# Kernel tuning notes

Hardware: AMD Instinct MI355X
Metric: run time of the kernel (lower is better)

## Reference

```python
import jax, jax.numpy as jnp
import numpy as np

NUM_FIELDS = 32
EMBED = 64
ATTN = 64
BATCH = 2048

# all field pairs (i < j), NC2 = 496
_ROW, _COL = np.triu_indices(NUM_FIELDS, k=1)
ROW_IDX = jnp.asarray(_ROW, dtype=jnp.int32)
COL_IDX = jnp.asarray(_COL, dtype=jnp.int32)


def setup_inputs() -> dict:
    key = jax.random.key(0)
    k0, k1, k2 = jax.random.split(key, 3)
    inputs = jax.random.normal(k0, (BATCH, NUM_FIELDS, EMBED), dtype=jnp.float32)
    # Linear init ~ U(-1/sqrt(fan_in), 1/sqrt(fan_in)) style scale
    W1 = jax.random.normal(k1, (EMBED, ATTN), dtype=jnp.float32) / jnp.sqrt(float(EMBED))
    b1 = jnp.zeros((ATTN,), dtype=jnp.float32)
    w2 = jax.random.normal(k2, (ATTN, 1), dtype=jnp.float32) / jnp.sqrt(float(ATTN))
    b2 = jnp.zeros((1,), dtype=jnp.float32)
    return {"inputs": inputs, "W1": W1, "b1": b1, "w2": w2, "b2": b2}


def reference(inputs, W1, b1, w2, b2):
    # inner: (B, P, E) pairwise elementwise products of field embeddings
    inner = inputs[:, ROW_IDX, :] * inputs[:, COL_IDX, :]
    # tiny 2-layer MLP attention: (B, P, E) -> (B, P, A) -> (B, P, 1)
    h = jax.nn.relu(jnp.einsum('bpe,ea->bpa', inner, W1) + b1)
    logits = jnp.einsum('bpa,ao->bpo', h, w2) + b2          # (B, P, 1)
    attn_scores = jax.nn.softmax(logits, axis=1)            # softmax over pair dim
    # softmax-weighted sum over pairs -> (B, E), then (B, 1, E)
    outputs = jnp.sum(attn_scores * inner, axis=1)
    return outputs[:, None, :], attn_scores
```

## Files before the change

### kernel.cpp

```cpp
#include <hip/hip_runtime.h>
#include <math.h>

#define NF 32
#define NE 64
#define NA 64
#define NP 496

typedef __attribute__((ext_vector_type(8))) _Float16 f16x8;
typedef __attribute__((ext_vector_type(4))) _Float16 f16x4;
typedef __attribute__((ext_vector_type(4))) float    f32x4;

#define W1T_S 72
#define XT_S  40
#define WT_S  40

__global__ __launch_bounds__(256, 4) void afm_fwd(
    const float* __restrict__ x,
    const float* __restrict__ W1,
    const float* __restrict__ b1,
    const float* __restrict__ w2,
    const float* __restrict__ b2,
    float* __restrict__ out,
    float* __restrict__ attn,
    int B)
{
    const int tid   = threadIdx.x;
    const int lane  = tid & 63;
    const int wv    = tid >> 6;
    const int smp   = wv >> 1;
    const int sub   = wv & 1;
    const int nlane = lane & 15;
    const int g     = lane >> 4;

    __shared__ __align__(16) _Float16 W1t[64][W1T_S];
    __shared__ __align__(16) _Float16 xh[2][8][NF][8];
    __shared__ __align__(16) _Float16 xT[2][NE][XT_S];
    __shared__ __align__(16) _Float16 Wt[2][NF][WT_S];
    __shared__ float s_l[2][NP];
    __shared__ unsigned short s_rc[512];

    {
        const int e = tid & 63, a0 = (tid >> 6) << 4;
        const float* wr = W1 + e * NA + a0;
        #pragma unroll
        for (int i = 0; i < 4; ++i) {
            const float4 v = *(const float4*)(wr + 4 * i);
            W1t[a0 + 4*i + 0][e] = (_Float16)v.x;
            W1t[a0 + 4*i + 1][e] = (_Float16)v.y;
            W1t[a0 + 4*i + 2][e] = (_Float16)v.z;
            W1t[a0 + 4*i + 3][e] = (_Float16)v.w;
        }
    }
    for (int p = tid; p < 512; p += 256) {
        const int pp = (p < NP) ? p : NP - 1;
        const float sq = sqrtf((float)(3969 - 8 * pp));
        int r = (int)((63.0f - sq) * 0.5f);
        int st = (r * (63 - r)) >> 1;
        if (pp < st) { --r; st = (r * (63 - r)) >> 1; }
        else { const int st2 = ((r + 1) * (62 - r)) >> 1; if (pp >= st2) { ++r; st = st2; } }
        const int c = pp - st + r + 1;
        s_rc[p] = (unsigned short)(r | (c << 8));
    }

    int b = blockIdx.x * 2 + smp;
    if (b >= B) b = B - 1;

    {
        unsigned int* wz = (unsigned int*)&Wt[smp][0][0];
        #pragma unroll
        for (int i = 0; i < 5; ++i) {
            const int idx = i * 64 + lane;
            if (idx < 320) wz[sub * 320 + idx] = 0u;
        }
    }

    const float* __restrict__ xb = x + (size_t)b * (NF * NE);
    {
        const int r  = sub * 16 + (lane >> 2);
        const int e0 = (lane & 3) << 4;
        #pragma unroll
        for (int i = 0; i < 4; ++i) {
            const int e = e0 + 4 * i;
            const float4 v = *(const float4*)(xb + r * NE + e);
            f16x4 hv = { (_Float16)v.x, (_Float16)v.y, (_Float16)v.z, (_Float16)v.w };
            *(f16x4*)&xh[smp][e >> 3][r][e & 7] = hv;
            xT[smp][e + 0][r] = hv[0];
            xT[smp][e + 1][r] = hv[1];
            xT[smp][e + 2][r] = hv[2];
            xT[smp][e + 3][r] = hv[3];
        }
    }
    __syncthreads();

    f16x8 w1f[2][4];
    #pragma unroll
    for (int s = 0; s < 2; ++s)
        #pragma unroll
        for (int mt = 0; mt < 4; ++mt)
            w1f[s][mt] = *(const f16x8*)&W1t[mt * 16 + nlane][s * 32 + g * 8];

    f32x4 b1q[4], w2q[4];
    #pragma unroll
    for (int mt = 0; mt < 4; ++mt) {
        b1q[mt] = *(const f32x4*)(b1 + mt * 16 + g * 4);
        w2q[mt] = *(const f32x4*)(w2 + mt * 16 + g * 4);
    }
    const float bias2 = b2[0];

    const int t_end = sub ? 31 : 16;
    #pragma unroll 2
    for (int t = sub * 16; t < t_end; ++t) {
        const int p0 = t << 4;
        const unsigned short rc = s_rc[p0 + nlane];
        const int r = rc & 255, c = rc >> 8;

        f16x8 af[2];
        #pragma unroll
        for (int s = 0; s < 2; ++s) {
            const f16x8 xr8 = *(const f16x8*)&xh[smp][4 * s + g][r][0];
            const f16x8 xc8 = *(const f16x8*)&xh[smp][4 * s + g][c][0];
            af[s] = xr8 * xc8;
        }
        f32x4 acc[4];
        #pragma unroll
        for (int mt = 0; mt < 4; ++mt) acc[mt] = b1q[mt];
        #pragma unroll
        for (int s = 0; s < 2; ++s)
            #pragma unroll
            for (int mt = 0; mt < 4; ++mt)
                acc[mt] = __builtin_amdgcn_mfma_f32_16x16x32_f16(w1f[s][mt], af[s], acc[mt], 0, 0, 0);

        float logit = 0.0f;
        #pragma unroll
        for (int mt = 0; mt < 4; ++mt) {
            logit = fmaf(fmaxf(acc[mt][0], 0.0f), w2q[mt][0], logit);
            logit = fmaf(fmaxf(acc[mt][1], 0.0f), w2q[mt][1], logit);
            logit = fmaf(fmaxf(acc[mt][2], 0.0f), w2q[mt][2], logit);
            logit = fmaf(fmaxf(acc[mt][3], 0.0f), w2q[mt][3], logit);
        }
        logit += __shfl_xor(logit, 16);
        logit += __shfl_xor(logit, 32);
        if (lane < 16) s_l[smp][p0 + lane] = logit + bias2;
    }
    __syncthreads();

    float lv[8], mx = -1e30f;
    #pragma unroll
    for (int k = 0; k < 8; ++k) {
        const int p = (k << 6) + lane;
        lv[k] = (p < NP) ? s_l[smp][p] : -1e30f;
        mx = fmaxf(mx, lv[k]);
    }
    #pragma unroll
    for (int off = 1; off < 64; off <<= 1) mx = fmaxf(mx, __shfl_xor(mx, off));

    float ev[8], se = 0.0f;
    #pragma unroll
    for (int k = 0; k < 8; ++k) {
        const int p = (k << 6) + lane;
        ev[k] = (p < NP) ? __expf(lv[k] - mx) : 0.0f;
        se += ev[k];
    }
    #pragma unroll
    for (int off = 1; off < 64; off <<= 1) se += __shfl_xor(se, off);
    const float inv = 1.0f / se;

    float* __restrict__ attn_b = attn + (size_t)b * NP;
    #pragma unroll
    for (int k = 0; k < 4; ++k) {
        const int kk = (sub << 2) + k;
        const int p = (kk << 6) + lane;
        if (p < NP) {
            const float w = ev[kk] * inv;
            attn_b[p] = w;
            const unsigned short rc = s_rc[p];
            const int r = rc & 255, c = rc >> 8;
            const _Float16 wh = (_Float16)w;
            Wt[smp][r][c] = wh;
            Wt[smp][c][r] = wh;
        }
    }
    __syncthreads();

    f16x8 wa[2], xbf[2];
    #pragma unroll
    for (int mt = 0; mt < 2; ++mt)
        wa[mt] = *(const f16x8*)&Wt[smp][mt * 16 + nlane][g * 8];
    #pragma unroll
    for (int j = 0; j < 2; ++j) {
        const int nt = 2 * sub + j;
        xbf[j] = *(const f16x8*)&xT[smp][nt * 16 + nlane][g * 8];
    }

    f32x4 y[2][2];
    #pragma unroll
    for (int mt = 0; mt < 2; ++mt)
        #pragma unroll
        for (int j = 0; j < 2; ++j) {
            y[mt][j] = (f32x4)0.0f;
            y[mt][j] = __builtin_amdgcn_mfma_f32_16x16x32_f16(wa[mt], xbf[j], y[mt][j], 0, 0, 0);
        }

    float po[2] = {0.f, 0.f};
    #pragma unroll
    for (int j = 0; j < 2; ++j) {
        const int nt = 2 * sub + j;
        #pragma unroll
        for (int mt = 0; mt < 2; ++mt) {
            const f16x4 xv = *(const f16x4*)&xT[smp][nt * 16 + nlane][mt * 16 + g * 4];
            po[j] += (float)xv[0] * y[mt][j][0];
            po[j] += (float)xv[1] * y[mt][j][1];
            po[j] += (float)xv[2] * y[mt][j][2];
            po[j] += (float)xv[3] * y[mt][j][3];
        }
        po[j] += __shfl_xor(po[j], 16);
        po[j] += __shfl_xor(po[j], 32);
    }
    if (lane < 16) {
        float* __restrict__ ob = out + (size_t)b * NE;
        #pragma unroll
        for (int j = 0; j < 2; ++j)
            ob[(2 * sub + j) * 16 + lane] = 0.5f * po[j];
    }
}

extern "C" void kernel_launch(void* const* d_in, const int* in_sizes, int n_in,
                              void* d_out, int out_size, void* d_ws, size_t ws_size,
                              hipStream_t stream) {
    const float* x  = (const float*)d_in[0];
    const float* W1 = (const float*)d_in[1];
    const float* b1 = (const float*)d_in[2];
    const float* w2 = (const float*)d_in[3];
    const float* b2 = (const float*)d_in[4];

    const int B = in_sizes[0] / (NF * NE);
    float* out_p  = (float*)d_out;
    float* attn_p = (float*)d_out + (size_t)B * NE;

    afm_fwd<<<(B + 1) / 2, 256, 0, stream>>>(x, W1, b1, w2, b2, out_p, attn_p, B);
}
```

Measured before the change: 23.38 us.

## Compute pair indices incrementally per lane and fully unroll the logit loop

Each lane now handles a contiguous run of 31 pairs. It computes its starting (row, col) once and advances it incrementally, so each iteration no longer reads the index table from shared memory. The loop is fully unrolled with a guard, MFMA issue priority is raised with s_setprio, and the w2 dot product is split into four independent accumulators for more ILP. The strided logit writes (31*lane) to shared memory may cause bank conflicts, and full unrolling increases code size and register pressure.

```diff
diff --git a/kernel.cpp b/kernel.cpp
--- a/kernel.cpp
+++ b/kernel.cpp
@@ -90,6 +90,18 @@
             xT[smp][e + 3][r] = hv[3];
         }
     }
+
+    int pr, pc;
+    {
+        const int p0 = 31 * nlane + 16 * sub;
+        const float sq = sqrtf((float)(3969 - 8 * p0));
+        int r = (int)((63.0f - sq) * 0.5f);
+        int st = (r * (63 - r)) >> 1;
+        if (p0 < st) { --r; st = (r * (63 - r)) >> 1; }
+        else { const int st2 = ((r + 1) * (62 - r)) >> 1; if (p0 >= st2) { ++r; st = st2; } }
+        pr = r;
+        pc = p0 - st + r + 1;
+    }
     __syncthreads();
 
     f16x8 w1f[2][4];
@@ -107,40 +119,45 @@
     }
     const float bias2 = b2[0];
 
-    const int t_end = sub ? 31 : 16;
-    #pragma unroll 2
-    for (int t = sub * 16; t < t_end; ++t) {
-        const int p0 = t << 4;
-        const unsigned short rc = s_rc[p0 + nlane];
-        const int r = rc & 255, c = rc >> 8;
-
-        f16x8 af[2];
-        #pragma unroll
-        for (int s = 0; s < 2; ++s) {
-            const f16x8 xr8 = *(const f16x8*)&xh[smp][4 * s + g][r][0];
-            const f16x8 xc8 = *(const f16x8*)&xh[smp][4 * s + g][c][0];
-            af[s] = xr8 * xc8;
-        }
-        f32x4 acc[4];
-        #pragma unroll
-        for (int mt = 0; mt < 4; ++mt) acc[mt] = b1q[mt];
-        #pragma unroll
-        for (int s = 0; s < 2; ++s)
-            #pragma unroll
-            for (int mt = 0; mt < 4; ++mt)
-                acc[mt] = __builtin_amdgcn_mfma_f32_16x16x32_f16(w1f[s][mt], af[s], acc[mt], 0, 0, 0);
-
-        float logit = 0.0f;
-        #pragma unroll
-        for (int mt = 0; mt < 4; ++mt) {
-            logit = fmaf(fmaxf(acc[mt][0], 0.0f), w2q[mt][0], logit);
-            logit = fmaf(fmaxf(acc[mt][1], 0.0f), w2q[mt][1], logit);
-            logit = fmaf(fmaxf(acc[mt][2], 0.0f), w2q[mt][2], logit);
-            logit = fmaf(fmaxf(acc[mt][3], 0.0f), w2q[mt][3], logit);
-        }
-        logit += __shfl_xor(logit, 16);
-        logit += __shfl_xor(logit, 32);
-        if (lane < 16) s_l[smp][p0 + lane] = logit + bias2;
+    #pragma unroll
+    for (int t = 0; t < 16; ++t) {
+        if (16 * sub + t < 31) {
+            f16x8 af[2];
+            #pragma unroll
+            for (int s = 0; s < 2; ++s) {
+                const f16x8 xr8 = *(const f16x8*)&xh[smp][4 * s + g][pr][0];
+                const f16x8 xc8 = *(const f16x8*)&xh[smp][4 * s + g][pc][0];
+                af[s] = xr8 * xc8;
+            }
+            f32x4 acc[4];
+            #pragma unroll
+            for (int mt = 0; mt < 4; ++mt) acc[mt] = b1q[mt];
+            __builtin_amdgcn_s_setprio(1);
+            #pragma unroll
+            for (int s = 0; s < 2; ++s)
+                #pragma unroll
+                for (int mt = 0; mt < 4; ++mt)
+                    acc[mt] = __builtin_amdgcn_mfma_f32_16x16x32_f16(w1f[s][mt], af[s], acc[mt], 0, 0, 0);
+            __builtin_amdgcn_s_setprio(0);
+
+            float pl0 = 0.f, pl1 = 0.f, pl2 = 0.f, pl3 = 0.f;
+            #pragma unroll
+            for (int mt = 0; mt < 4; ++mt) {
+                pl0 = fmaf(fmaxf(acc[mt][0], 0.0f), w2q[mt][0], pl0);
+                pl1 = fmaf(fmaxf(acc[mt][1], 0.0f), w2q[mt][1], pl1);
+                pl2 = fmaf(fmaxf(acc[mt][2], 0.0f), w2q[mt][2], pl2);
+                pl3 = fmaf(fmaxf(acc[mt][3], 0.0f), w2q[mt][3], pl3);
+            }
+            float logit = (pl0 + pl1) + (pl2 + pl3);
+            logit += __shfl_xor(logit, 16);
+            logit += __shfl_xor(logit, 32);
+            if (lane < 16) s_l[smp][31 * lane + 16 * sub + t] = logit + bias2;
+
+            ++pc;
+            const int wrap = (pc >= 32) ? 1 : 0;
+            pr += wrap;
+            pc = wrap ? (pr + 1) : pc;
+        }
     }
     __syncthreads();
 
```

After: 22.43 us. 4.0% less time.
